# Performance work log

Hardware: AMD Instinct MI355X
Metric: run time of the kernel (lower is better)

The kernel has to match this reference:

```python
import jax, jax.numpy as jnp
import numpy as np

B, S, H, V = 2, 2048, 4096, 32000

def setup_inputs() -> dict:
    key = jax.random.key(0)
    k1, k2, k3, k4 = jax.random.split(key, 4)
    return {
        "hidden_states": jax.random.normal(k1, (B, S, H), dtype=jnp.float32),
        "head_weight": jax.random.normal(k2, (V, H), dtype=jnp.float32) * 0.02,
        "labels": jax.random.randint(k3, (B, S), 0, V, dtype=jnp.int64),
        "loss_weight": jax.random.uniform(k4, (B, S), dtype=jnp.float32),
        "grad_accumulation_steps": 1,
    }

def reference(hidden_states, head_weight, labels, loss_weight, grad_accumulation_steps):
    # logits = F.linear(hidden_states, head_weight)  -> [B, S, V]
    logits = jnp.einsum("bsh,vh->bsv", hidden_states, head_weight)
    flat_logits = logits.reshape(-1, logits.shape[-1])   # [T, V]
    flat_labels = labels.reshape(-1)                      # [T]
    # per-token cross entropy (reduction='none'): -log_softmax[label]
    logz = jax.nn.logsumexp(flat_logits, axis=-1)         # [T]
    picked = jnp.take_along_axis(flat_logits, flat_labels[:, None], axis=-1)[:, 0]
    per_tok = logz - picked                               # [T]
    w = loss_weight.reshape(-1)
    w_sum = jnp.sum(w)  # all_reduce(mean) is identity on one device
    loss = jnp.sum(per_tok * w) / (w_sum + 1e-8)
    loss = loss / grad_accumulation_steps
    return loss
```

## Files before the change

### kernel.cpp

```cpp
#include <hip/hip_runtime.h>
#include <hip/hip_bf16.h>

#define T_TOK 4096
#define HDIM  4096
#define VOCAB 32000
#define BM8   256
#define BN8   256
#define BKB   128
#define NT_K  (HDIM / BKB)
#define NTT8  (T_TOK / BM8)
#define NVT8  (VOCAB / BN8)

typedef float f32x4 __attribute__((ext_vector_type(4)));
typedef int   i32x4 __attribute__((ext_vector_type(4)));

#define GLD_LDS16(gsrc, ldst)                                                  \
  __builtin_amdgcn_global_load_lds(                                            \
      (const __attribute__((address_space(1))) void*)(gsrc),                   \
      (__attribute__((address_space(3))) void*)(ldst), 16, 0, 0)

__global__ __launch_bounds__(256) void ce_quant_38766374814398(
    const float* __restrict__ in, signed char* __restrict__ out,
    float* __restrict__ scales)
{
  const int row = blockIdx.x;
  const int tid = threadIdx.x;
  const float* src = in + (size_t)row * HDIM;

  f32x4 v[4];
  float mx = 0.f;
#pragma unroll
  for (int j = 0; j < 4; ++j) {
    v[j] = *(const f32x4*)(src + tid * 16 + j * 4);
    mx = fmaxf(mx, fmaxf(fmaxf(fabsf(v[j][0]), fabsf(v[j][1])),
                         fmaxf(fabsf(v[j][2]), fabsf(v[j][3]))));
  }
#pragma unroll
  for (int off = 1; off < 64; off <<= 1)
    mx = fmaxf(mx, __shfl_xor(mx, off, 64));
  __shared__ float wm4[4];
  if ((tid & 63) == 0) wm4[tid >> 6] = mx;
  __syncthreads();
  mx = fmaxf(fmaxf(wm4[0], wm4[1]), fmaxf(wm4[2], wm4[3]));
  mx = fmaxf(mx, 1e-20f);
  const float inv = 127.0f / mx;
  if (tid == 0) scales[row] = mx / 127.0f;

  i32x4 o;
#pragma unroll
  for (int j = 0; j < 4; ++j) {
    int b0 = min(127, max(-127, __float2int_rn(v[j][0] * inv))) & 0xff;
    int b1 = min(127, max(-127, __float2int_rn(v[j][1] * inv))) & 0xff;
    int b2 = min(127, max(-127, __float2int_rn(v[j][2] * inv))) & 0xff;
    int b3 = min(127, max(-127, __float2int_rn(v[j][3] * inv))) & 0xff;
    o[j] = b0 | (b1 << 8) | (b2 << 16) | (b3 << 24);
  }
  *(i32x4*)(out + (size_t)row * HDIM + tid * 16) = o;
}

__global__ __launch_bounds__(512, 2) void ce_gemm8q_38766374814398(
    const signed char* __restrict__ Aq, const signed char* __restrict__ Wq,
    const float* __restrict__ s_t, const float* __restrict__ s_v,
    const int* __restrict__ labels, float* __restrict__ sumexp,
    float* __restrict__ picked)
{
  __shared__ __attribute__((aligned(16))) signed char sA0[BM8 * BKB];
  __shared__ __attribute__((aligned(16))) signed char sA1[BM8 * BKB];
  __shared__ __attribute__((aligned(16))) signed char sB0[BN8 * BKB];
  __shared__ __attribute__((aligned(16))) signed char sB1[BN8 * BKB];

  const int tid  = threadIdx.x;
  const int lane = tid & 63;
  const int wid  = tid >> 6;
  const int wm   = wid >> 2;
  const int wn   = wid & 3;

  const int bid = blockIdx.x;
  const int tt  = (bid & 7) * 2 + ((bid >> 3) & 1);
  const int vt  = (bid >> 3) >> 1;

  const signed char* gA = Aq + (size_t)tt * BM8 * HDIM;
  const signed char* gB = Wq + (size_t)vt * BN8 * HDIM;

  const int kswB = (((lane & 7) ^ (lane >> 3)) << 4);

#define STAGE_A(arr, kt, half)                                                 \
  do {                                                                         \
    _Pragma("unroll")                                                          \
    for (int call = 0; call < 2; ++call) {                                     \
      const int chunk = call * 16 + (half) * 8 + wid;                          \
      const int row   = chunk * 8 + (lane >> 3);                               \
      GLD_LDS16(gA + (size_t)row * HDIM + (size_t)(kt) * BKB + kswB,           \
                &(arr)[chunk * 1024]);                                         \
    }                                                                          \
  } while (0)

#define STAGE_B(arr, kt, half)                                                 \
  do {                                                                         \
    _Pragma("unroll")                                                          \
    for (int call = 0; call < 2; ++call) {                                     \
      const int chunk = (half) * 16 + call * 8 + wid;                          \
      const int row   = chunk * 8 + (lane >> 3);                               \
      GLD_LDS16(gB + (size_t)row * HDIM + (size_t)(kt) * BKB + kswB,           \
                &(arr)[chunk * 1024]);                                         \
    }                                                                          \
  } while (0)

#define B_READ(arr)                                                            \
  _Pragma("unroll")                                                            \
  for (int ni = 0; ni < 4; ++ni)                                               \
    _Pragma("unroll")                                                          \
    for (int s = 0; s < 2; ++s) {                                              \
      const int br   = wn * 64 + ni * 16 + (lane & 15);                        \
      const int cidx = s * 4 + (lane >> 4);                                    \
      bfrag[ni][s] =                                                           \
          *(const i32x4*)&(arr)[br * BKB + ((cidx ^ (br & 7)) << 4)];          \
    }

#define A_READ_H(dst, h, arr)                                                  \
  _Pragma("unroll")                                                            \
  for (int b = 0; b < 4; ++b)                                                  \
    _Pragma("unroll")                                                          \
    for (int s = 0; s < 2; ++s) {                                              \
      const int ar   = wm * 128 + (h) * 64 + b * 16 + (lane & 15);             \
      const int cidx = s * 4 + (lane >> 4);                                    \
      dst[b][s] =                                                              \
          *(const i32x4*)&(arr)[ar * BKB + ((cidx ^ (ar & 7)) << 4)];          \
    }

#define PHASE_SYNC()                                                           \
  do {                                                                         \
    __builtin_amdgcn_sched_barrier(0);                                         \
    __builtin_amdgcn_s_barrier();                                              \
    __builtin_amdgcn_sched_barrier(0);                                         \
  } while (0)

#define DO_MFMA_H(h, FR)                                                       \
  do {                                                                         \
    __builtin_amdgcn_s_setprio(1);                                             \
    _Pragma("unroll")                                                          \
    for (int b = 0; b < 4; ++b)                                                \
      _Pragma("unroll")                                                        \
      for (int ni = 0; ni < 4; ++ni)                                           \
        _Pragma("unroll")                                                      \
        for (int s = 0; s < 2; ++s)                                            \
          acc[(h) * 4 + b][ni] = __builtin_amdgcn_mfma_i32_16x16x64_i8(        \
              FR[b][s], bfrag[ni][s], acc[(h) * 4 + b][ni], 0, 0, 0);          \
    __builtin_amdgcn_s_setprio(0);                                             \
  } while (0)

#define TILE(t, CA, CB, OA)                                                    \
  do {                                                                         \
    i32x4 bfrag[4][2];                                                         \
    i32x4 aq[4][2];                                                            \
              \
    B_READ(CB);                                                                \
    A_READ_H(aq, 0, CA);                                                       \
    if ((t) + 1 < NT_K) STAGE_A(OA, (t) + 1, 1);                               \
    PHASE_SYNC();                                                              \
    DO_MFMA_H(0, aq);                                                          \
    __builtin_amdgcn_sched_barrier(0);                                         \
    __builtin_amdgcn_s_barrier();                                              \
      \
    A_READ_H(aq, 1, CA);                                                       \
    if ((t) + 2 < NT_K) {                                                      \
      STAGE_B(CB, (t) + 2, 0);                                                 \
      STAGE_B(CB, (t) + 2, 1);                                                 \
      STAGE_A(CA, (t) + 2, 0);                                                 \
    }                                                                          \
    PHASE_SYNC();                                                              \
    DO_MFMA_H(1, aq);                                                          \
    __builtin_amdgcn_sched_barrier(0);                                         \
    if ((t) + 2 < NT_K)      asm volatile("s_waitcnt vmcnt(6)" ::: "memory");  \
    else if ((t) + 1 < NT_K) asm volatile("s_waitcnt vmcnt(0)" ::: "memory");  \
    __builtin_amdgcn_s_barrier();                                              \
  } while (0)

  i32x4 acc[8][4];
#pragma unroll
  for (int i = 0; i < 8; ++i)
#pragma unroll
    for (int j = 0; j < 4; ++j)
      acc[i][j] = (i32x4){0, 0, 0, 0};

  STAGE_B(sB0, 0, 0);
  STAGE_B(sB0, 0, 1);
  STAGE_A(sA0, 0, 0);
  STAGE_A(sA0, 0, 1);
  STAGE_B(sB1, 1, 0);
  STAGE_B(sB1, 1, 1);
  STAGE_A(sA1, 1, 0);
  asm volatile("s_waitcnt vmcnt(6)" ::: "memory");
  __builtin_amdgcn_s_barrier();

  for (int t = 0; t < NT_K; t += 2) {
    TILE(t,     sA0, sB0, sA1);
    TILE(t + 1, sA1, sB1, sA0);
  }

  const int row0 = tt * BM8 + wm * 128 + ((lane >> 4) << 2);
  const int col0 = vt * BN8 + wn * 64 + (lane & 15);
  float sv[4];
#pragma unroll
  for (int ni = 0; ni < 4; ++ni) sv[ni] = s_v[col0 + ni * 16];
#pragma unroll
  for (int mi = 0; mi < 8; ++mi) {
#pragma unroll
    for (int r = 0; r < 4; ++r) {
      const int row = row0 + mi * 16 + r;
      const int lab = labels[row];
      const float st = s_t[row];
      float se = 0.f;
#pragma unroll
      for (int ni = 0; ni < 4; ++ni) {
        const float lg = (float)acc[mi][ni][r] * st * sv[ni];
        se += expf(lg);
        if (col0 + ni * 16 == lab) picked[row] = lg;
      }
      se += __shfl_xor(se, 1, 64);
      se += __shfl_xor(se, 2, 64);
      se += __shfl_xor(se, 4, 64);
      se += __shfl_xor(se, 8, 64);
      if ((lane & 15) == 0) atomicAdd(&sumexp[row], se);
    }
  }
#undef STAGE_A
#undef STAGE_B
#undef B_READ
#undef A_READ_H
#undef PHASE_SYNC
#undef DO_MFMA_H
#undef TILE
}

typedef __bf16 bf16x8 __attribute__((ext_vector_type(8)));
#define BM 128
#define BN 128
#define BK 64
#define NTT (T_TOK / BM)
#define NVT (VOCAB / BN)
__global__ __launch_bounds__(256) void ce_fused_gemm_38766374814398(
    const float* __restrict__ hs, const float* __restrict__ wt,
    const int* __restrict__ labels, float* __restrict__ sumexp,
    float* __restrict__ picked)
{
  __shared__ __bf16 lA[BM * BK];
  __shared__ __bf16 lB[BN * BK];

  const int tid  = threadIdx.x;
  const int lane = tid & 63;
  const int wid  = tid >> 6;
  const int wm   = wid >> 1;
  const int wn   = wid & 1;

  const int bid = blockIdx.x;
  const int sw  = (bid & 7) * (NTT * NVT / 8) + (bid >> 3);
  const int vt  = sw >> 5;
  const int tt  = sw & 31;

  const float* gA = hs + (size_t)tt * BM * HDIM;
  const float* gB = wt + (size_t)vt * BN * HDIM;

  f32x4 acc[4][4];
#pragma unroll
  for (int i = 0; i < 4; ++i)
#pragma unroll
    for (int j = 0; j < 4; ++j)
      acc[i][j] = (f32x4){0.f, 0.f, 0.f, 0.f};

  for (int kt = 0; kt < HDIM / BK; ++kt) {
    const int kbase = kt * BK;
#pragma unroll
    for (int t = 0; t < 4; ++t) {
      const int c   = t * 256 + tid;
      const int row = c >> 3;
      const int kc  = (c & 7) << 3;
      const float* g = gA + (size_t)row * HDIM + kbase + kc;
      f32x4 p0 = *(const f32x4*)g;
      f32x4 p1 = *(const f32x4*)(g + 4);
      bf16x8 v;
      v[0] = (__bf16)p0[0]; v[1] = (__bf16)p0[1]; v[2] = (__bf16)p0[2]; v[3] = (__bf16)p0[3];
      v[4] = (__bf16)p1[0]; v[5] = (__bf16)p1[1]; v[6] = (__bf16)p1[2]; v[7] = (__bf16)p1[3];
      *(bf16x8*)&lA[(row << 6) + ((((c & 7) ^ row) & 7) << 3)] = v;
    }
#pragma unroll
    for (int t = 0; t < 4; ++t) {
      const int c   = t * 256 + tid;
      const int row = c >> 3;
      const int kc  = (c & 7) << 3;
      const float* g = gB + (size_t)row * HDIM + kbase + kc;
      f32x4 p0 = *(const f32x4*)g;
      f32x4 p1 = *(const f32x4*)(g + 4);
      bf16x8 v;
      v[0] = (__bf16)p0[0]; v[1] = (__bf16)p0[1]; v[2] = (__bf16)p0[2]; v[3] = (__bf16)p0[3];
      v[4] = (__bf16)p1[0]; v[5] = (__bf16)p1[1]; v[6] = (__bf16)p1[2]; v[7] = (__bf16)p1[3];
      *(bf16x8*)&lB[(row << 6) + ((((c & 7) ^ row) & 7) << 3)] = v;
    }
    __syncthreads();

#pragma unroll
    for (int kk = 0; kk < 2; ++kk) {
      bf16x8 af[4], bfr[4];
      const int slot = kk * 4 + (lane >> 4);
#pragma unroll
      for (int mi = 0; mi < 4; ++mi) {
        const int ar = wm * 64 + mi * 16 + (lane & 15);
        af[mi] = *(const bf16x8*)&lA[(ar << 6) + (((slot ^ ar) & 7) << 3)];
      }
#pragma unroll
      for (int ni = 0; ni < 4; ++ni) {
        const int br = wn * 64 + ni * 16 + (lane & 15);
        bfr[ni] = *(const bf16x8*)&lB[(br << 6) + (((slot ^ br) & 7) << 3)];
      }
#pragma unroll
      for (int mi = 0; mi < 4; ++mi)
#pragma unroll
        for (int ni = 0; ni < 4; ++ni)
          acc[mi][ni] = __builtin_amdgcn_mfma_f32_16x16x32_bf16(af[mi], bfr[ni], acc[mi][ni], 0, 0, 0);
    }
    __syncthreads();
  }

  const int row0 = tt * BM + wm * 64 + ((lane >> 4) << 2);
  const int col0 = vt * BN + wn * 64 + (lane & 15);
#pragma unroll
  for (int mi = 0; mi < 4; ++mi) {
#pragma unroll
    for (int r = 0; r < 4; ++r) {
      const int row = row0 + mi * 16 + r;
      const int lab = labels[row];
      float se = 0.f;
#pragma unroll
      for (int ni = 0; ni < 4; ++ni) {
        const float lg = acc[mi][ni][r];
        se += expf(lg);
        if (col0 + ni * 16 == lab) picked[row] = lg;
      }
      se += __shfl_xor(se, 1, 64);
      se += __shfl_xor(se, 2, 64);
      se += __shfl_xor(se, 4, 64);
      se += __shfl_xor(se, 8, 64);
      if ((lane & 15) == 0) atomicAdd(&sumexp[row], se);
    }
  }
}

__global__ __launch_bounds__(256) void ce_reduce_38766374814398(
    const float* __restrict__ sumexp, const float* __restrict__ picked,
    const float* __restrict__ lw, const int* __restrict__ gas,
    float* __restrict__ out)
{
  __shared__ float sl[4], sww[4];
  const int tid = threadIdx.x;
  float accl = 0.f, accw = 0.f;
  for (int t = tid; t < T_TOK; t += 256) {
    const float w = lw[t];
    accl += w * (logf(sumexp[t]) - picked[t]);
    accw += w;
  }
#pragma unroll
  for (int off = 32; off > 0; off >>= 1) {
    accl += __shfl_down(accl, off, 64);
    accw += __shfl_down(accw, off, 64);
  }
  if ((tid & 63) == 0) { sl[tid >> 6] = accl; sww[tid >> 6] = accw; }
  __syncthreads();
  if (tid == 0) {
    float L = 0.f, W = 0.f;
#pragma unroll
    for (int i = 0; i < 4; ++i) { L += sl[i]; W += sww[i]; }
    out[0] = L / (W + 1e-8f) / (float)gas[0];
  }
}

extern "C" void kernel_launch(void* const* d_in, const int* in_sizes, int n_in,
                              void* d_out, int out_size, void* d_ws, size_t ws_size,
                              hipStream_t stream) {
  const float* hs     = (const float*)d_in[0];
  const float* wt     = (const float*)d_in[1];
  const int*   labels = (const int*)d_in[2];
  const float* lw     = (const float*)d_in[3];
  const int*   gas    = (const int*)d_in[4];

  const size_t off_sumexp = 0;
  const size_t off_picked = 16384;
  const size_t off_st     = 32768;
  const size_t off_sv     = 49152;
  const size_t off_hq     = 177152;
  const size_t off_wq     = 177152 + (size_t)T_TOK * HDIM;
  const size_t need       = off_wq + (size_t)VOCAB * HDIM;

  float* sumexp = (float*)((char*)d_ws + off_sumexp);
  float* picked = (float*)((char*)d_ws + off_picked);

  hipMemsetAsync(sumexp, 0, T_TOK * sizeof(float), stream);

  if (ws_size >= need) {
    float* s_t = (float*)((char*)d_ws + off_st);
    float* s_v = (float*)((char*)d_ws + off_sv);
    signed char* hq = (signed char*)d_ws + off_hq;
    signed char* wq = (signed char*)d_ws + off_wq;

    ce_quant_38766374814398<<<dim3(T_TOK), dim3(256), 0, stream>>>(hs, hq, s_t);
    ce_quant_38766374814398<<<dim3(VOCAB), dim3(256), 0, stream>>>(wt, wq, s_v);
    ce_gemm8q_38766374814398<<<dim3(NTT8 * NVT8), dim3(512), 0, stream>>>(
        hq, wq, s_t, s_v, labels, sumexp, picked);
  } else {
    ce_fused_gemm_38766374814398<<<dim3(NTT * NVT), dim3(256), 0, stream>>>(
        hs, wt, labels, sumexp, picked);
  }
  ce_reduce_38766374814398<<<dim3(1), dim3(256), 0, stream>>>(
      sumexp, picked, lw, gas, (float*)d_out);
}
```

Baseline: 804.4 us.

## Prefetch next tile's A/B register fragments during current MFMA phase

Restructures the int8 GEMM main loop so LDS reads of the next K-tile's A half and B fragments are issued before the second MFMA half of the current tile, using double-buffered register fragments (afA/afB, bfrA/bfrB). Global-to-LDS staging for A and B is reordered and the vmcnt waits are adjusted to match. The aim is to hide LDS read latency behind MFMA work. In exchange it raises VGPR pressure, which could lower occupancy or cause spills, and it relies on tight vmcnt accounting for correctness.

Measured after the change: 2.979 ms. +270.4%, slower.

```diff
diff --git a/kernel.cpp b/kernel.cpp
--- a/kernel.cpp
+++ b/kernel.cpp
@@ -106,14 +106,14 @@
     }                                                                          \
   } while (0)
 
-#define B_READ(arr)                                                            \
+#define B_READ(dst, arr)                                                       \
   _Pragma("unroll")                                                            \
   for (int ni = 0; ni < 4; ++ni)                                               \
     _Pragma("unroll")                                                          \
     for (int s = 0; s < 2; ++s) {                                              \
       const int br   = wn * 64 + ni * 16 + (lane & 15);                        \
       const int cidx = s * 4 + (lane >> 4);                                    \
-      bfrag[ni][s] =                                                           \
+      dst[ni][s] =                                                             \
           *(const i32x4*)&(arr)[br * BKB + ((cidx ^ (br & 7)) << 4)];          \
     }
 
@@ -135,7 +135,7 @@
     __builtin_amdgcn_sched_barrier(0);                                         \
   } while (0)
 
-#define DO_MFMA_H(h, FR)                                                       \
+#define DO_MFMA(h, AF, BF)                                                     \
   do {                                                                         \
     __builtin_amdgcn_s_setprio(1);                                             \
     _Pragma("unroll")                                                          \
@@ -145,34 +145,31 @@
         _Pragma("unroll")                                                      \
         for (int s = 0; s < 2; ++s)                                            \
           acc[(h) * 4 + b][ni] = __builtin_amdgcn_mfma_i32_16x16x64_i8(        \
-              FR[b][s], bfrag[ni][s], acc[(h) * 4 + b][ni], 0, 0, 0);          \
+              AF[b][s], BF[ni][s], acc[(h) * 4 + b][ni], 0, 0, 0);             \
     __builtin_amdgcn_s_setprio(0);                                             \
   } while (0)
 
-#define TILE(t, CA, CB, OA)                                                    \
+#define TILE(t, CA, CB, OA, OB, BCUR, BNXT)                                    \
   do {                                                                         \
-    i32x4 bfrag[4][2];                                                         \
-    i32x4 aq[4][2];                                                            \
-              \
-    B_READ(CB);                                                                \
-    A_READ_H(aq, 0, CA);                                                       \
-    if ((t) + 1 < NT_K) STAGE_A(OA, (t) + 1, 1);                               \
+                \
+    A_READ_H(afB, 1, CA);                                                      \
+    if ((t) + 2 < NT_K) { STAGE_B(CB, (t) + 2, 0); STAGE_B(CB, (t) + 2, 1); }  \
     PHASE_SYNC();                                                              \
-    DO_MFMA_H(0, aq);                                                          \
+    DO_MFMA(0, afA, BCUR);                                                     \
     __builtin_amdgcn_sched_barrier(0);                                         \
     __builtin_amdgcn_s_barrier();                                              \
-      \
-    A_READ_H(aq, 1, CA);                                                       \
-    if ((t) + 2 < NT_K) {                                                      \
-      STAGE_B(CB, (t) + 2, 0);                                                 \
-      STAGE_B(CB, (t) + 2, 1);                                                 \
-      STAGE_A(CA, (t) + 2, 0);                                                 \
+                                                     \
+    if ((t) + 2 < NT_K) asm volatile("s_waitcnt vmcnt(4)" ::: "memory");       \
+    else                asm volatile("s_waitcnt vmcnt(0)" ::: "memory");       \
+    __builtin_amdgcn_sched_barrier(0);                                         \
+    if ((t) + 1 < NT_K) {                                                      \
+      A_READ_H(afA, 0, OA);                                                    \
+      B_READ(BNXT, OB);                                                        \
     }                                                                          \
+    if ((t) + 2 < NT_K) { STAGE_A(CA, (t) + 2, 0); STAGE_A(CA, (t) + 2, 1); }  \
     PHASE_SYNC();                                                              \
-    DO_MFMA_H(1, aq);                                                          \
+    DO_MFMA(1, afB, BCUR);                                                     \
     __builtin_amdgcn_sched_barrier(0);                                         \
-    if ((t) + 2 < NT_K)      asm volatile("s_waitcnt vmcnt(6)" ::: "memory");  \
-    else if ((t) + 1 < NT_K) asm volatile("s_waitcnt vmcnt(0)" ::: "memory");  \
     __builtin_amdgcn_s_barrier();                                              \
   } while (0)
 
@@ -183,19 +180,24 @@
     for (int j = 0; j < 4; ++j)
       acc[i][j] = (i32x4){0, 0, 0, 0};
 
-  STAGE_B(sB0, 0, 0);
-  STAGE_B(sB0, 0, 1);
-  STAGE_A(sA0, 0, 0);
-  STAGE_A(sA0, 0, 1);
-  STAGE_B(sB1, 1, 0);
-  STAGE_B(sB1, 1, 1);
-  STAGE_A(sA1, 1, 0);
-  asm volatile("s_waitcnt vmcnt(6)" ::: "memory");
+  i32x4 afA[4][2];
+  i32x4 afB[4][2];
+  i32x4 bfrA[4][2];
+  i32x4 bfrB[4][2];
+
+  STAGE_B(sB0, 0, 0);  STAGE_B(sB0, 0, 1);
+  STAGE_A(sA0, 0, 0);  STAGE_A(sA0, 0, 1);
+  STAGE_B(sB1, 1, 0);  STAGE_B(sB1, 1, 1);
+  STAGE_A(sA1, 1, 0);  STAGE_A(sA1, 1, 1);
+  asm volatile("s_waitcnt vmcnt(8)" ::: "memory");
   __builtin_amdgcn_s_barrier();
-
+  A_READ_H(afA, 0, sA0);
+  B_READ(bfrA, sB0);
+  __builtin_amdgcn_sched_barrier(0);
+  __builtin_amdgcn_s_barrier();
   for (int t = 0; t < NT_K; t += 2) {
-    TILE(t,     sA0, sB0, sA1);
-    TILE(t + 1, sA1, sB1, sA0);
+    TILE(t,     sA0, sB0, sA1, sB1, bfrA, bfrB);
+    TILE(t + 1, sA1, sB1, sA0, sB0, bfrB, bfrA);
   }
 
   const int row0 = tt * BM8 + wm * 128 + ((lane >> 4) << 2);
@@ -229,7 +231,7 @@
 #undef B_READ
 #undef A_READ_H
 #undef PHASE_SYNC
-#undef DO_MFMA_H
+#undef DO_MFMA
 #undef TILE
 }
 
```
